# Performance work log

Hardware: AMD Instinct MI355X
Metric: run time of the kernel (lower is better)

The kernel has to match this reference:

```python
import jax, jax.numpy as jnp
import numpy as np
import math

N_HEADS = 16
D_MODEL = 1024
D_FF = 4096
MAX_REL = 32  # max_relative_position
LN_EPS = 1e-5


def _layernorm(x, g, b):
    m = jnp.mean(x, axis=-1, keepdims=True)
    v = jnp.var(x, axis=-1, keepdims=True)
    return (x - m) * jax.lax.rsqrt(v + LN_EPS) * g + b


def setup_inputs() -> dict:
    key = jax.random.key(0)
    ks = jax.random.split(key, 12)
    D, F = D_MODEL, D_FF
    gain = 1.0 / math.sqrt(2.0)
    xav = lambda k, o, i, g=1.0: jax.random.uniform(k, (o, i), jnp.float32, -1.0, 1.0) * (g * math.sqrt(6.0 / (o + i)))
    return {
        "x": jax.random.normal(ks[0], (2, 2048, D), jnp.float32),
        "wq": xav(ks[1], D, D, gain),
        "wk": xav(ks[2], D, D, gain),
        "wv": xav(ks[3], D, D, gain),
        "wo": xav(ks[4], D, D, gain),
        "wo_b": jnp.zeros((D,), jnp.float32),
        "rel_tab": jax.random.normal(ks[5], (2 * MAX_REL - 1, N_HEADS), jnp.float32) * 0.02,
        "ln1_g": jnp.ones((D,), jnp.float32),
        "ln1_b": jnp.zeros((D,), jnp.float32),
        "ln2_g": jnp.ones((D,), jnp.float32),
        "ln2_b": jnp.zeros((D,), jnp.float32),
        "w1": xav(ks[6], F, D),
        "b1": jnp.zeros((F,), jnp.float32),
        "w2": xav(ks[7], D, F),
        "b2": jnp.zeros((D,), jnp.float32),
    }


def reference(x, wq, wk, wv, wo, wo_b, rel_tab, ln1_g, ln1_b, ln2_g, ln2_b, w1, b1, w2, b2):
    B, S, D = x.shape
    H = N_HEADS
    dk = D // H

    def proj(w):  # torch Linear: x @ w.T, then split heads -> [B,H,S,dk]
        return (x @ w.T).reshape(B, S, H, dk).transpose(0, 2, 1, 3)

    q, k, v = proj(wq), proj(wk), proj(wv)

    # Rotary embeddings (per-head dim), exact interleave-to-block formula from source
    t = jnp.arange(S, dtype=jnp.float32)
    inv_freq = 1.0 / (10000.0 ** (jnp.arange(0, dk, 2, dtype=jnp.float32) / dk))
    freqs = t[:, None] * inv_freq[None, :]  # [S, dk/2]
    cos, sin = jnp.cos(freqs), jnp.sin(freqs)

    def rope(z):
        z1, z2 = z[..., ::2], z[..., 1::2]  # [B,H,S,dk/2]
        return jnp.concatenate([z1 * cos - z2 * sin, z1 * sin + z2 * cos], axis=-1)

    q, k = rope(q), rope(k)

    # Manual attention with learned relative-position bias
    scores = jnp.einsum("bhqd,bhkd->bhqk", q, k) / math.sqrt(dk)
    rel = jnp.arange(S)[:, None] - jnp.arange(S)[None, :]
    rel = jnp.clip(rel, -(MAX_REL - 1), MAX_REL - 1) + (MAX_REL - 1)
    bias = rel_tab[rel]  # [S,S,H]
    scores = scores + jnp.transpose(bias, (2, 0, 1))[None]  # [1,H,S,S]
    attn = jax.nn.softmax(scores, axis=-1)
    o = jnp.einsum("bhqk,bhkd->bhqd", attn, v).transpose(0, 2, 1, 3).reshape(B, S, D)
    o = o @ wo.T + wo_b

    # Post-norm residual block
    h = _layernorm(x + o, ln1_g, ln1_b)
    f = jax.nn.gelu(h @ w1.T + b1, approximate=False) @ w2.T + b2
    return _layernorm(h + f, ln2_g, ln2_b)
```

## Files before the change

### kernel.cpp

```cpp
#include <hip/hip_runtime.h>
#include <stdint.h>

#define MB (1ull << 20)
typedef unsigned short u16;
typedef __attribute__((ext_vector_type(8))) short bf16x8;
typedef __attribute__((ext_vector_type(4))) float f32x4;

__device__ __forceinline__ float b2f(u16 u) {
  union { unsigned int i; float f; } c; c.i = ((unsigned int)u) << 16; return c.f;
}
__device__ __forceinline__ u16 f2b(float f) {
  union { float f; unsigned int i; } c; c.f = f;
  unsigned int r = c.i + 0x7fffu + ((c.i >> 16) & 1u);
  return (u16)(r >> 16);
}
__device__ __forceinline__ void gload16(const void* g, void* l) {
  __builtin_amdgcn_global_load_lds(
      (const __attribute__((address_space(1))) void*)g,
      (__attribute__((address_space(3))) void*)l, 16, 0, 0);
}

__global__ __launch_bounds__(256) void f2b_kernel(const float* __restrict__ in,
                                                  u16* __restrict__ out, int n) {
  int i = (blockIdx.x * 256 + threadIdx.x) * 4;
  if (i + 3 >= n) { for (int j = 0; j < 4 && i + j < n; j++) out[i + j] = f2b(in[i + j]); return; }
  float4 v = *(const float4*)(in + i);
  uint2 o;
  o.x = (unsigned)f2b(v.x) | ((unsigned)f2b(v.y) << 16);
  o.y = (unsigned)f2b(v.z) | ((unsigned)f2b(v.w) << 16);
  *(uint2*)(out + i) = o;
}

template<int EPI, int BM>
__global__ __launch_bounds__(256) void gemm_bt(
    const u16* __restrict__ A, const u16* __restrict__ B,
    u16* __restrict__ C, const float* __restrict__ bias,
    int M, int N, int K)
{
  constexpr int MT = BM / 32;
  __shared__ __align__(16) u16 As[BM * 64];
  __shared__ __align__(16) u16 Bs[128 * 64];
  const int tid = threadIdx.x;
  const int lane = tid & 63, wave = tid >> 6;
  const int lr = lane & 15, lg = lane >> 4;
  const int wm = wave >> 1, wn = wave & 1;

  const int nwg = gridDim.x * gridDim.y;
  const int id = blockIdx.y * gridDim.x + blockIdx.x;
  const int nid = (id & 7) * (nwg >> 3) + (id >> 3);
  const int bx = nid % gridDim.x, by = nid / gridDim.x;

  const int srow = tid >> 3;
  const int scsw = ((tid & 7) * 8) ^ ((srow & 7) << 3);
  const size_t abase = (size_t)(by * BM + srow) * K + scsw;
  const size_t bbase = (size_t)(bx * 128 + srow) * K + scsw;

  int aoff[MT][2], boff[4][2];
  #pragma unroll
  for (int mt = 0; mt < MT; mt++) {
    int row = wm * (BM / 2) + mt * 16 + lr;
    #pragma unroll
    for (int kk = 0; kk < 2; kk++)
      aoff[mt][kk] = row * 64 + ((kk * 32 + lg * 8) ^ ((row & 7) << 3));
  }
  #pragma unroll
  for (int nt = 0; nt < 4; nt++) {
    int row = wn * 64 + nt * 16 + lr;
    #pragma unroll
    for (int kk = 0; kk < 2; kk++)
      boff[nt][kk] = row * 64 + ((kk * 32 + lg * 8) ^ ((row & 7) << 3));
  }

  f32x4 acc[MT][4];
  #pragma unroll
  for (int i = 0; i < MT; i++)
    #pragma unroll
    for (int j = 0; j < 4; j++) acc[i][j] = (f32x4){0.f, 0.f, 0.f, 0.f};

  for (int k0 = 0; k0 < K; k0 += 64) {
    __syncthreads();
    #pragma unroll
    for (int h = 0; h < MT; h++)
      gload16(A + abase + (size_t)(h * 32) * K + k0, &As[h * 2048 + tid * 8]);
    #pragma unroll
    for (int h = 0; h < 4; h++)
      gload16(B + bbase + (size_t)(h * 32) * K + k0, &Bs[h * 2048 + tid * 8]);
    __syncthreads();
    #pragma unroll
    for (int kk = 0; kk < 2; kk++) {
      bf16x8 af[MT], bfr[4];
      #pragma unroll
      for (int mt = 0; mt < MT; mt++) af[mt] = *(const bf16x8*)&As[aoff[mt][kk]];
      #pragma unroll
      for (int nt = 0; nt < 4; nt++) bfr[nt] = *(const bf16x8*)&Bs[boff[nt][kk]];
      #pragma unroll
      for (int mt = 0; mt < MT; mt++)
        #pragma unroll
        for (int nt = 0; nt < 4; nt++)
          acc[mt][nt] = __builtin_amdgcn_mfma_f32_16x16x32_bf16(af[mt], bfr[nt], acc[mt][nt], 0, 0, 0);
    }
  }

  #pragma unroll
  for (int mt = 0; mt < MT; mt++)
    #pragma unroll
    for (int nt = 0; nt < 4; nt++) {
      const int row = by * BM + wm * (BM / 2) + mt * 16 + lg * 4;
      const int col = bx * 128 + wn * 64 + nt * 16 + lr;
      const float bv = (EPI >= 1) ? bias[col] : 0.f;
      #pragma unroll
      for (int r = 0; r < 4; r++) {
        float x = acc[mt][nt][r] + bv;
        if (EPI == 2) x = 0.5f * x * (1.f + erff(x * 0.70710678118654752f));
        C[(size_t)(row + r) * N + col] = f2b(x);
      }
    }
}

__global__ __launch_bounds__(256) void rope_kernel(
    const u16* __restrict__ qp, const u16* __restrict__ kp, int stride,
    u16* __restrict__ qr, u16* __restrict__ kr)
{
  const int gid = blockIdx.x * 4 + (threadIdx.x >> 6);
  const int lane = threadIdx.x & 63;
  const int s = gid & 2047;
  const int bh = gid >> 11;
  const int h = bh & 15, b = bh >> 4;
  const int j = lane & 31;
  const float inv = exp2f(-(float)j * (13.287712379549449f / 32.0f));
  float sn, cs;
  sincosf((float)s * inv, &sn, &cs);
  const size_t base = (size_t)(b * 2048 + s) * stride + h * 64;
  float q1 = b2f(qp[base + 2 * j]), q2 = b2f(qp[base + 2 * j + 1]);
  float k1 = b2f(kp[base + 2 * j]), k2 = b2f(kp[base + 2 * j + 1]);
  float qo = (lane < 32) ? (q1 * cs - q2 * sn) : (q1 * sn + q2 * cs);
  float ko = (lane < 32) ? (k1 * cs - k2 * sn) : (k1 * sn + k2 * cs);
  qr[(size_t)gid * 64 + lane] = f2b(qo);
  kr[(size_t)gid * 64 + lane] = f2b(ko);
}

__global__ __launch_bounds__(256) void vtrans_kernel(
    const u16* __restrict__ vp, int stride, u16* __restrict__ vT)
{
  __shared__ u16 t[64][65];
  const int sc = blockIdx.x & 31;
  const int bh = blockIdx.x >> 5;
  const int h = bh & 15, b = bh >> 4;
  const int tid = threadIdx.x;
  #pragma unroll
  for (int i = 0; i < 16; i++) {
    int idx = i * 256 + tid;
    int sl = idx >> 6, d = idx & 63;
    t[sl][d] = vp[(size_t)(b * 2048 + sc * 64 + sl) * stride + h * 64 + d];
  }
  __syncthreads();
  #pragma unroll
  for (int i = 0; i < 16; i++) {
    int idx = i * 256 + tid;
    int d = idx >> 6, sl = idx & 63;
    vT[((size_t)bh * 64 + d) * 2048 + sc * 64 + sl] = t[sl][d];
  }
}

__global__ __launch_bounds__(256) void attn_kernel(
    const u16* __restrict__ qr, const u16* __restrict__ kr,
    const u16* __restrict__ vT, const float* __restrict__ rel_tab,
    u16* __restrict__ o)
{
  __shared__ __align__(16) u16 Ks[64 * 64];
  __shared__ __align__(16) u16 Vs[64 * 64];
  __shared__ __align__(16) u16 Ps[4][16 * 64];
  __shared__ float bias_s[64];

  const int tid = threadIdx.x;
  const int lane = tid & 63, wave = tid >> 6;
  const int lr = lane & 15, lg = lane >> 4;

  const int id = blockIdx.x;
  const int nid = (id & 7) * 128 + (id >> 3);
  const int bh = nid >> 5, qc = nid & 31;
  const int h = bh & 15, b = bh >> 4;
  const int q0 = qc * 64 + wave * 16;

  if (tid < 63) bias_s[tid] = rel_tab[tid * 16 + h] * 1.4426950408889634f;

  const u16* qb = qr + (size_t)bh * 2048 * 64;
  const u16* kb = kr + (size_t)bh * 2048 * 64;
  const u16* vb = vT + (size_t)bh * 64 * 2048;

  bf16x8 qf[2];
  qf[0] = *(const bf16x8*)(qb + (size_t)(q0 + lr) * 64 + lg * 8);
  qf[1] = *(const bf16x8*)(qb + (size_t)(q0 + lr) * 64 + 32 + lg * 8);

  const int srow = tid >> 3;
  const int scsw = ((tid & 7) * 8) ^ ((srow & 7) << 3);

  int koff[4][2], poff[2];
  #pragma unroll
  for (int nt = 0; nt < 4; nt++)
    #pragma unroll
    for (int ks = 0; ks < 2; ks++)
      koff[nt][ks] = (nt * 16 + lr) * 64 + ((ks * 32 + lg * 8) ^ ((lr & 7) << 3));
  #pragma unroll
  for (int ks = 0; ks < 2; ks++)
    poff[ks] = lr * 64 + ((ks * 32 + lg * 8) ^ ((lr & 7) << 3));

  float mrow[4], lpart[4];
  #pragma unroll
  for (int r = 0; r < 4; r++) { mrow[r] = -1e30f; lpart[r] = 0.f; }
  f32x4 oacc[4];
  #pragma unroll
  for (int nt = 0; nt < 4; nt++) oacc[nt] = (f32x4){0.f, 0.f, 0.f, 0.f};

  const float SC = 0.18033688011112042f;

  for (int kc = 0; kc < 32; kc++) {
    const int k0 = kc * 64;
    __syncthreads();
    #pragma unroll
    for (int hh = 0; hh < 2; hh++) {
      gload16(kb + (size_t)(k0 + hh * 32 + srow) * 64 + scsw, &Ks[hh * 2048 + tid * 8]);
      gload16(vb + (size_t)(hh * 32 + srow) * 2048 + k0 + scsw, &Vs[hh * 2048 + tid * 8]);
    }
    __syncthreads();

    f32x4 sacc[4];
    #pragma unroll
    for (int nt = 0; nt < 4; nt++) sacc[nt] = (f32x4){0.f, 0.f, 0.f, 0.f};
    #pragma unroll
    for (int ks = 0; ks < 2; ks++)
      #pragma unroll
      for (int nt = 0; nt < 4; nt++) {
        bf16x8 kf = *(const bf16x8*)&Ks[koff[nt][ks]];
        sacc[nt] = __builtin_amdgcn_mfma_f32_16x16x32_bf16(qf[ks], kf, sacc[nt], 0, 0, 0);
      }

    float sv[4][4];
    const int dmin = q0 - k0 - 63, dmax = q0 + 15 - k0;
    if (dmin >= 31 || dmax <= -31) {
      const float c = bias_s[dmin >= 31 ? 62 : 0];
      #pragma unroll
      for (int nt = 0; nt < 4; nt++)
        #pragma unroll
        for (int r = 0; r < 4; r++) sv[nt][r] = sacc[nt][r] * SC + c;
    } else {
      #pragma unroll
      for (int nt = 0; nt < 4; nt++)
        #pragma unroll
        for (int r = 0; r < 4; r++) {
          int d = (q0 + lg * 4 + r) - (k0 + nt * 16 + lr);
          d = d < -31 ? -31 : (d > 31 ? 31 : d);
          sv[nt][r] = sacc[nt][r] * SC + bias_s[d + 31];
        }
    }

    float rm[4];
    #pragma unroll
    for (int r = 0; r < 4; r++) {
      float m = fmaxf(fmaxf(sv[0][r], sv[1][r]), fmaxf(sv[2][r], sv[3][r]));
      m = fmaxf(m, __shfl_xor(m, 1));
      m = fmaxf(m, __shfl_xor(m, 2));
      m = fmaxf(m, __shfl_xor(m, 4));
      m = fmaxf(m, __shfl_xor(m, 8));
      rm[r] = m;
    }
    int defer = (rm[0] <= mrow[0] + 11.5f) & (rm[1] <= mrow[1] + 11.5f) &
                (rm[2] <= mrow[2] + 11.5f) & (rm[3] <= mrow[3] + 11.5f);
    if (!__all(defer)) {
      #pragma unroll
      for (int r = 0; r < 4; r++) {
        float mnew = fmaxf(mrow[r], rm[r]);
        float sc = exp2f(mrow[r] - mnew);
        lpart[r] *= sc;
        #pragma unroll
        for (int nt = 0; nt < 4; nt++) oacc[nt][r] *= sc;
        mrow[r] = mnew;
      }
    }
    #pragma unroll
    for (int r = 0; r < 4; r++) {
      const int prow = lg * 4 + r;
      const int sw = (prow & 7) << 3;
      #pragma unroll
      for (int nt = 0; nt < 4; nt++) {
        float p = exp2f(sv[nt][r] - mrow[r]);
        lpart[r] += p;
        Ps[wave][prow * 64 + ((nt * 16 + lr) ^ sw)] = f2b(p);
      }
    }
    #pragma unroll
    for (int ks = 0; ks < 2; ks++) {
      bf16x8 pf = *(const bf16x8*)&Ps[wave][poff[ks]];
      #pragma unroll
      for (int nt = 0; nt < 4; nt++) {
        bf16x8 vf = *(const bf16x8*)&Vs[koff[nt][ks]];
        oacc[nt] = __builtin_amdgcn_mfma_f32_16x16x32_bf16(pf, vf, oacc[nt], 0, 0, 0);
      }
    }
  }

  #pragma unroll
  for (int r = 0; r < 4; r++) {
    float l = lpart[r];
    l += __shfl_xor(l, 1); l += __shfl_xor(l, 2);
    l += __shfl_xor(l, 4); l += __shfl_xor(l, 8);
    lpart[r] = 1.0f / l;
  }
  #pragma unroll
  for (int nt = 0; nt < 4; nt++)
    #pragma unroll
    for (int r = 0; r < 4; r++) {
      int qa = q0 + lg * 4 + r;
      int d = nt * 16 + lr;
      o[(size_t)(b * 2048 + qa) * 1024 + h * 64 + d] = f2b(oacc[nt][r] * lpart[r]);
    }
}

__global__ __launch_bounds__(256) void ln1_kernel(
    const float* __restrict__ x, const u16* __restrict__ ao,
    const float* __restrict__ g, const float* __restrict__ bta,
    u16* __restrict__ hb)
{
  const int row = blockIdx.x, tid = threadIdx.x;
  const int wave = tid >> 6, lane = tid & 63;
  float v[4]; float s = 0.f, s2 = 0.f;
  #pragma unroll
  for (int j = 0; j < 4; j++) {
    int c = tid + j * 256;
    float t = x[(size_t)row * 1024 + c] + b2f(ao[(size_t)row * 1024 + c]);
    v[j] = t; s += t; s2 += t * t;
  }
  #pragma unroll
  for (int off = 32; off >= 1; off >>= 1) { s += __shfl_down(s, off); s2 += __shfl_down(s2, off); }
  __shared__ float rs[4], rs2[4];
  if (lane == 0) { rs[wave] = s; rs2[wave] = s2; }
  __syncthreads();
  s = rs[0] + rs[1] + rs[2] + rs[3];
  s2 = rs2[0] + rs2[1] + rs2[2] + rs2[3];
  float mean = s * (1.f / 1024.f);
  float var = s2 * (1.f / 1024.f) - mean * mean;
  float inv = rsqrtf(var + 1e-5f);
  #pragma unroll
  for (int j = 0; j < 4; j++) {
    int c = tid + j * 256;
    hb[(size_t)row * 1024 + c] = f2b((v[j] - mean) * inv * g[c] + bta[c]);
  }
}

__global__ __launch_bounds__(256) void ln2_kernel(
    const u16* __restrict__ hb, const u16* __restrict__ fb,
    const float* __restrict__ g, const float* __restrict__ bta,
    float* __restrict__ out)
{
  const int row = blockIdx.x, tid = threadIdx.x;
  const int wave = tid >> 6, lane = tid & 63;
  float v[4]; float s = 0.f, s2 = 0.f;
  #pragma unroll
  for (int j = 0; j < 4; j++) {
    int c = tid + j * 256;
    float t = b2f(hb[(size_t)row * 1024 + c]) + b2f(fb[(size_t)row * 1024 + c]);
    v[j] = t; s += t; s2 += t * t;
  }
  #pragma unroll
  for (int off = 32; off >= 1; off >>= 1) { s += __shfl_down(s, off); s2 += __shfl_down(s2, off); }
  __shared__ float rs[4], rs2[4];
  if (lane == 0) { rs[wave] = s; rs2[wave] = s2; }
  __syncthreads();
  s = rs[0] + rs[1] + rs[2] + rs[3];
  s2 = rs2[0] + rs2[1] + rs2[2] + rs2[3];
  float mean = s * (1.f / 1024.f);
  float var = s2 * (1.f / 1024.f) - mean * mean;
  float inv = rsqrtf(var + 1e-5f);
  #pragma unroll
  for (int j = 0; j < 4; j++) {
    int c = tid + j * 256;
    out[(size_t)row * 1024 + c] = (v[j] - mean) * inv * g[c] + bta[c];
  }
}

extern "C" void kernel_launch(void* const* d_in, const int* in_sizes, int n_in,
                              void* d_out, int out_size, void* d_ws, size_t ws_size,
                              hipStream_t stream)
{
  const float* x    = (const float*)d_in[0];
  const float* wq   = (const float*)d_in[1];
  const float* wk   = (const float*)d_in[2];
  const float* wv   = (const float*)d_in[3];
  const float* wo   = (const float*)d_in[4];
  const float* wo_b = (const float*)d_in[5];
  const float* rel  = (const float*)d_in[6];
  const float* ln1g = (const float*)d_in[7];
  const float* ln1b = (const float*)d_in[8];
  const float* ln2g = (const float*)d_in[9];
  const float* ln2b = (const float*)d_in[10];
  const float* w1   = (const float*)d_in[11];
  const float* b1   = (const float*)d_in[12];
  const float* w2   = (const float*)d_in[13];
  const float* b2   = (const float*)d_in[14];
  float* out = (float*)d_out;
  char* w = (char*)d_ws;

  if (ws_size < (size_t)90 * MB) return;

  u16* xb    = (u16*)(w + 0 * MB);
  u16* wqkvb = (u16*)(w + 8 * MB);
  u16* wob   = (u16*)(w + 14 * MB);
  u16* w1b   = (u16*)(w + 16 * MB);
  u16* w2b   = (u16*)(w + 24 * MB);
  u16* qkv   = (u16*)(w + 32 * MB);
  u16* ob    = (u16*)(w + 32 * MB);
  u16* ao    = (u16*)(w + 40 * MB);
  u16* hb    = (u16*)(w + 48 * MB);
  u16* qrb   = (u16*)(w + 56 * MB);
  u16* krb   = (u16*)(w + 64 * MB);
  u16* vTb   = (u16*)(w + 72 * MB);
  u16* gb    = (u16*)(w + 56 * MB);
  u16* fb    = (u16*)(w + 0 * MB);

  const int M = 4096, D = 1024, F = 4096;

  f2b_kernel<<<dim3(M * D / 1024), 256, 0, stream>>>(x, xb, M * D);
  f2b_kernel<<<dim3(D * D / 1024), 256, 0, stream>>>(wq, wqkvb, D * D);
  f2b_kernel<<<dim3(D * D / 1024), 256, 0, stream>>>(wk, wqkvb + D * D, D * D);
  f2b_kernel<<<dim3(D * D / 1024), 256, 0, stream>>>(wv, wqkvb + 2 * D * D, D * D);
  f2b_kernel<<<dim3(D * D / 1024), 256, 0, stream>>>(wo, wob, D * D);
  f2b_kernel<<<dim3(F * D / 1024), 256, 0, stream>>>(w1, w1b, F * D);
  f2b_kernel<<<dim3(D * F / 1024), 256, 0, stream>>>(w2, w2b, D * F);

  gemm_bt<0, 128><<<dim3(3 * D / 128, M / 128), 256, 0, stream>>>(xb, wqkvb, qkv, nullptr, M, 3 * D, D);

  rope_kernel<<<dim3(16384), 256, 0, stream>>>(qkv, qkv + 1024, 3 * D, qrb, krb);
  vtrans_kernel<<<dim3(1024), 256, 0, stream>>>(qkv + 2048, 3 * D, vTb);

  attn_kernel<<<dim3(1024), 256, 0, stream>>>(qrb, krb, vTb, rel, ob);

  gemm_bt<1, 64><<<dim3(D / 128, M / 64), 256, 0, stream>>>(ob, wob, ao, wo_b, M, D, D);

  ln1_kernel<<<dim3(M), 256, 0, stream>>>(x, ao, ln1g, ln1b, hb);

  gemm_bt<2, 128><<<dim3(F / 128, M / 128), 256, 0, stream>>>(hb, w1b, gb, b1, M, F, D);

  gemm_bt<1, 64><<<dim3(D / 128, M / 64), 256, 0, stream>>>(gb, w2b, fb, b2, M, D, F);

  ln2_kernel<<<dim3(M), 256, 0, stream>>>(hb, fb, ln2g, ln2b, out);
}
```

Baseline: 311.3 us.

## Double-buffer attention K/V, keep P in registers, fuse casts, precompute RoPE table

The attention kernel now double-buffers K/V tiles in LDS, prefetching the next chunk while computing the current one. It computes the transposed score tile so each lane owns one query row, which makes the per-row max and sum scalars. P is packed with v_cvt_pk_bf16_f32 and passed to the PV MFMA through ds_bpermute instead of an LDS round trip, with s_setprio around the MFMA sections. Separately, the seven fp32-to-bf16 conversions are merged into one launch and RoPE cos/sin come from a precomputed table, with paired 32-bit loads. This trades more LDS per block and lane shuffles for fewer barriers and fewer LDS writes; the attention loop drops the second __syncthreads, and it is not obvious that the async global_load_lds prefetch is guaranteed complete before the next iteration reads it.

```diff
diff --git a/kernel.cpp b/kernel.cpp
--- a/kernel.cpp
+++ b/kernel.cpp
@@ -20,15 +20,37 @@
       (__attribute__((address_space(3))) void*)l, 16, 0, 0);
 }
 
-__global__ __launch_bounds__(256) void f2b_kernel(const float* __restrict__ in,
-                                                  u16* __restrict__ out, int n) {
-  int i = (blockIdx.x * 256 + threadIdx.x) * 4;
-  if (i + 3 >= n) { for (int j = 0; j < 4 && i + j < n; j++) out[i + j] = f2b(in[i + j]); return; }
-  float4 v = *(const float4*)(in + i);
-  uint2 o;
-  o.x = (unsigned)f2b(v.x) | ((unsigned)f2b(v.y) << 16);
-  o.y = (unsigned)f2b(v.z) | ((unsigned)f2b(v.w) << 16);
-  *(uint2*)(out + i) = o;
+__global__ __launch_bounds__(256) void f2b_all(
+    const float* __restrict__ x, const float* __restrict__ wq, const float* __restrict__ wk,
+    const float* __restrict__ wv, const float* __restrict__ wo, const float* __restrict__ w1,
+    const float* __restrict__ w2,
+    u16* __restrict__ xb, u16* __restrict__ wqkvb, u16* __restrict__ wob,
+    u16* __restrict__ w1b, u16* __restrict__ w2b)
+{
+  int bid = blockIdx.x;
+  const float* src; u16* dst;
+  if (bid < 4096)       { src = x;  dst = xb; }
+  else if (bid < 5120)  { src = wq; dst = wqkvb;           bid -= 4096; }
+  else if (bid < 6144)  { src = wk; dst = wqkvb + 1048576; bid -= 5120; }
+  else if (bid < 7168)  { src = wv; dst = wqkvb + 2097152; bid -= 6144; }
+  else if (bid < 8192)  { src = wo; dst = wob;             bid -= 7168; }
+  else if (bid < 12288) { src = w1; dst = w1b;             bid -= 8192; }
+  else                  { src = w2; dst = w2b;             bid -= 12288; }
+  int i = (bid * 256 + threadIdx.x) * 4;
+  float4 v = *(const float4*)(src + i);
+  uint2 ov;
+  ov.x = (unsigned)f2b(v.x) | ((unsigned)f2b(v.y) << 16);
+  ov.y = (unsigned)f2b(v.z) | ((unsigned)f2b(v.w) << 16);
+  *(uint2*)(dst + i) = ov;
+}
+
+__global__ __launch_bounds__(256) void rope_tab_kernel(float2* __restrict__ tab) {
+  int idx = blockIdx.x * 256 + threadIdx.x;
+  int s = idx >> 5, j = idx & 31;
+  float inv = exp2f(-(float)j * (13.287712379549449f / 32.0f));
+  float sn, cs;
+  sincosf((float)s * inv, &sn, &cs);
+  tab[idx] = make_float2(cs, sn);
 }
 
 template<int EPI, int BM>
@@ -119,7 +141,7 @@
 
 __global__ __launch_bounds__(256) void rope_kernel(
     const u16* __restrict__ qp, const u16* __restrict__ kp, int stride,
-    u16* __restrict__ qr, u16* __restrict__ kr)
+    const float2* __restrict__ tab, u16* __restrict__ qr, u16* __restrict__ kr)
 {
   const int gid = blockIdx.x * 4 + (threadIdx.x >> 6);
   const int lane = threadIdx.x & 63;
@@ -127,12 +149,13 @@
   const int bh = gid >> 11;
   const int h = bh & 15, b = bh >> 4;
   const int j = lane & 31;
-  const float inv = exp2f(-(float)j * (13.287712379549449f / 32.0f));
-  float sn, cs;
-  sincosf((float)s * inv, &sn, &cs);
+  float2 t = tab[s * 32 + j];
+  const float cs = t.x, sn = t.y;
   const size_t base = (size_t)(b * 2048 + s) * stride + h * 64;
-  float q1 = b2f(qp[base + 2 * j]), q2 = b2f(qp[base + 2 * j + 1]);
-  float k1 = b2f(kp[base + 2 * j]), k2 = b2f(kp[base + 2 * j + 1]);
+  unsigned int qv = *(const unsigned int*)(qp + base + 2 * j);
+  unsigned int kv = *(const unsigned int*)(kp + base + 2 * j);
+  float q1 = b2f((u16)qv), q2 = b2f((u16)(qv >> 16));
+  float k1 = b2f((u16)kv), k2 = b2f((u16)(kv >> 16));
   float qo = (lane < 32) ? (q1 * cs - q2 * sn) : (q1 * sn + q2 * cs);
   float ko = (lane < 32) ? (k1 * cs - k2 * sn) : (k1 * sn + k2 * cs);
   qr[(size_t)gid * 64 + lane] = f2b(qo);
@@ -167,9 +190,8 @@
     const u16* __restrict__ vT, const float* __restrict__ rel_tab,
     u16* __restrict__ o)
 {
-  __shared__ __align__(16) u16 Ks[64 * 64];
-  __shared__ __align__(16) u16 Vs[64 * 64];
-  __shared__ __align__(16) u16 Ps[4][16 * 64];
+  __shared__ __align__(16) u16 Ks[2][64 * 64];
+  __shared__ __align__(16) u16 Vs[2][64 * 64];
   __shared__ float bias_s[64];
 
   const int tid = threadIdx.x;
@@ -195,125 +217,144 @@
   const int srow = tid >> 3;
   const int scsw = ((tid & 7) * 8) ^ ((srow & 7) << 3);
 
-  int koff[4][2], poff[2];
+  int koff[4][2];
   #pragma unroll
   for (int nt = 0; nt < 4; nt++)
     #pragma unroll
     for (int ks = 0; ks < 2; ks++)
       koff[nt][ks] = (nt * 16 + lr) * 64 + ((ks * 32 + lg * 8) ^ ((lr & 7) << 3));
-  #pragma unroll
-  for (int ks = 0; ks < 2; ks++)
-    poff[ks] = lr * 64 + ((ks * 32 + lg * 8) ^ ((lr & 7) << 3));
-
-  float mrow[4], lpart[4];
-  #pragma unroll
-  for (int r = 0; r < 4; r++) { mrow[r] = -1e30f; lpart[r] = 0.f; }
+
+  #pragma unroll
+  for (int hh = 0; hh < 2; hh++) {
+    gload16(kb + (size_t)(hh * 32 + srow) * 64 + scsw, &Ks[0][hh * 2048 + tid * 8]);
+    gload16(vb + (size_t)(hh * 32 + srow) * 2048 + scsw, &Vs[0][hh * 2048 + tid * 8]);
+  }
+
+  float mrow = -1e30f, lpart = 0.f;
   f32x4 oacc[4];
   #pragma unroll
   for (int nt = 0; nt < 4; nt++) oacc[nt] = (f32x4){0.f, 0.f, 0.f, 0.f};
 
   const float SC = 0.18033688011112042f;
-
+  const int idx_lo = 4 * (lr + 16 * ((lg & 1) * 2));
+  const int idx_hi = idx_lo + 64;
+  const bool hiSel = (lg >= 2);
+
+  int cur = 0;
   for (int kc = 0; kc < 32; kc++) {
     const int k0 = kc * 64;
     __syncthreads();
-    #pragma unroll
-    for (int hh = 0; hh < 2; hh++) {
-      gload16(kb + (size_t)(k0 + hh * 32 + srow) * 64 + scsw, &Ks[hh * 2048 + tid * 8]);
-      gload16(vb + (size_t)(hh * 32 + srow) * 2048 + k0 + scsw, &Vs[hh * 2048 + tid * 8]);
-    }
-    __syncthreads();
+    if (kc < 31) {
+      const int kn = k0 + 64;
+      #pragma unroll
+      for (int hh = 0; hh < 2; hh++) {
+        gload16(kb + (size_t)(kn + hh * 32 + srow) * 64 + scsw, &Ks[cur ^ 1][hh * 2048 + tid * 8]);
+        gload16(vb + (size_t)(hh * 32 + srow) * 2048 + kn + scsw, &Vs[cur ^ 1][hh * 2048 + tid * 8]);
+      }
+    }
+    const u16* Kc = Ks[cur];
+    const u16* Vc = Vs[cur];
 
     f32x4 sacc[4];
     #pragma unroll
     for (int nt = 0; nt < 4; nt++) sacc[nt] = (f32x4){0.f, 0.f, 0.f, 0.f};
+    __builtin_amdgcn_s_setprio(1);
     #pragma unroll
     for (int ks = 0; ks < 2; ks++)
       #pragma unroll
       for (int nt = 0; nt < 4; nt++) {
-        bf16x8 kf = *(const bf16x8*)&Ks[koff[nt][ks]];
-        sacc[nt] = __builtin_amdgcn_mfma_f32_16x16x32_bf16(qf[ks], kf, sacc[nt], 0, 0, 0);
+        bf16x8 kf = *(const bf16x8*)&Kc[koff[nt][ks]];
+        sacc[nt] = __builtin_amdgcn_mfma_f32_16x16x32_bf16(kf, qf[ks], sacc[nt], 0, 0, 0);
       }
-
-    float sv[4][4];
+    __builtin_amdgcn_s_setprio(0);
+
+    float p[4][4];
     const int dmin = q0 - k0 - 63, dmax = q0 + 15 - k0;
     if (dmin >= 31 || dmax <= -31) {
       const float c = bias_s[dmin >= 31 ? 62 : 0];
       #pragma unroll
       for (int nt = 0; nt < 4; nt++)
         #pragma unroll
-        for (int r = 0; r < 4; r++) sv[nt][r] = sacc[nt][r] * SC + c;
+        for (int r = 0; r < 4; r++) p[nt][r] = sacc[nt][r] * SC + c;
     } else {
       #pragma unroll
       for (int nt = 0; nt < 4; nt++)
         #pragma unroll
         for (int r = 0; r < 4; r++) {
-          int d = (q0 + lg * 4 + r) - (k0 + nt * 16 + lr);
+          int d = (q0 + lr) - (k0 + nt * 16 + lg * 4 + r);
           d = d < -31 ? -31 : (d > 31 ? 31 : d);
-          sv[nt][r] = sacc[nt][r] * SC + bias_s[d + 31];
+          p[nt][r] = sacc[nt][r] * SC + bias_s[d + 31];
         }
     }
 
-    float rm[4];
-    #pragma unroll
-    for (int r = 0; r < 4; r++) {
-      float m = fmaxf(fmaxf(sv[0][r], sv[1][r]), fmaxf(sv[2][r], sv[3][r]));
-      m = fmaxf(m, __shfl_xor(m, 1));
-      m = fmaxf(m, __shfl_xor(m, 2));
-      m = fmaxf(m, __shfl_xor(m, 4));
-      m = fmaxf(m, __shfl_xor(m, 8));
-      rm[r] = m;
-    }
-    int defer = (rm[0] <= mrow[0] + 11.5f) & (rm[1] <= mrow[1] + 11.5f) &
-                (rm[2] <= mrow[2] + 11.5f) & (rm[3] <= mrow[3] + 11.5f);
-    if (!__all(defer)) {
-      #pragma unroll
-      for (int r = 0; r < 4; r++) {
-        float mnew = fmaxf(mrow[r], rm[r]);
-        float sc = exp2f(mrow[r] - mnew);
-        lpart[r] *= sc;
-        #pragma unroll
-        for (int nt = 0; nt < 4; nt++) oacc[nt][r] *= sc;
-        mrow[r] = mnew;
+    float rm = p[0][0];
+    #pragma unroll
+    for (int nt = 0; nt < 4; nt++)
+      #pragma unroll
+      for (int r = 0; r < 4; r++) rm = fmaxf(rm, p[nt][r]);
+    rm = fmaxf(rm, __shfl_xor(rm, 16));
+    rm = fmaxf(rm, __shfl_xor(rm, 32));
+
+    if (!__all(rm <= mrow + 11.5f)) {
+      float mnew = fmaxf(mrow, rm);
+      float sc = exp2f(mrow - mnew);
+      lpart *= sc;
+      #pragma unroll
+      for (int nt = 0; nt < 4; nt++) oacc[nt] *= sc;
+      mrow = mnew;
+    }
+
+    unsigned int pk[4][2];
+    #pragma unroll
+    for (int nt = 0; nt < 4; nt++)
+      #pragma unroll
+      for (int i = 0; i < 2; i++) {
+        float pa = exp2f(p[nt][2 * i] - mrow);
+        float pb = exp2f(p[nt][2 * i + 1] - mrow);
+        lpart += pa + pb;
+        unsigned int pr;
+        asm("v_cvt_pk_bf16_f32 %0, %1, %2" : "=v"(pr) : "v"(pa), "v"(pb));
+        pk[nt][i] = pr;
       }
-    }
-    #pragma unroll
-    for (int r = 0; r < 4; r++) {
-      const int prow = lg * 4 + r;
-      const int sw = (prow & 7) << 3;
+
+    __builtin_amdgcn_s_setprio(1);
+    #pragma unroll
+    for (int ks = 0; ks < 2; ks++) {
+      int w0a = __builtin_amdgcn_ds_bpermute(idx_lo, (int)pk[ks * 2][0]);
+      int w0b = __builtin_amdgcn_ds_bpermute(idx_lo, (int)pk[ks * 2 + 1][0]);
+      int w1a = __builtin_amdgcn_ds_bpermute(idx_lo, (int)pk[ks * 2][1]);
+      int w1b = __builtin_amdgcn_ds_bpermute(idx_lo, (int)pk[ks * 2 + 1][1]);
+      int w2a = __builtin_amdgcn_ds_bpermute(idx_hi, (int)pk[ks * 2][0]);
+      int w2b = __builtin_amdgcn_ds_bpermute(idx_hi, (int)pk[ks * 2 + 1][0]);
+      int w3a = __builtin_amdgcn_ds_bpermute(idx_hi, (int)pk[ks * 2][1]);
+      int w3b = __builtin_amdgcn_ds_bpermute(idx_hi, (int)pk[ks * 2 + 1][1]);
+      int4 bw;
+      bw.x = hiSel ? w0b : w0a;
+      bw.y = hiSel ? w1b : w1a;
+      bw.z = hiSel ? w2b : w2a;
+      bw.w = hiSel ? w3b : w3a;
+      bf16x8 pf = *(bf16x8*)&bw;
       #pragma unroll
       for (int nt = 0; nt < 4; nt++) {
-        float p = exp2f(sv[nt][r] - mrow[r]);
-        lpart[r] += p;
-        Ps[wave][prow * 64 + ((nt * 16 + lr) ^ sw)] = f2b(p);
+        bf16x8 vf = *(const bf16x8*)&Vc[koff[nt][ks]];
+        oacc[nt] = __builtin_amdgcn_mfma_f32_16x16x32_bf16(vf, pf, oacc[nt], 0, 0, 0);
       }
     }
-    #pragma unroll
-    for (int ks = 0; ks < 2; ks++) {
-      bf16x8 pf = *(const bf16x8*)&Ps[wave][poff[ks]];
-      #pragma unroll
-      for (int nt = 0; nt < 4; nt++) {
-        bf16x8 vf = *(const bf16x8*)&Vs[koff[nt][ks]];
-        oacc[nt] = __builtin_amdgcn_mfma_f32_16x16x32_bf16(pf, vf, oacc[nt], 0, 0, 0);
-      }
-    }
-  }
-
-  #pragma unroll
-  for (int r = 0; r < 4; r++) {
-    float l = lpart[r];
-    l += __shfl_xor(l, 1); l += __shfl_xor(l, 2);
-    l += __shfl_xor(l, 4); l += __shfl_xor(l, 8);
-    lpart[r] = 1.0f / l;
-  }
-  #pragma unroll
-  for (int nt = 0; nt < 4; nt++)
-    #pragma unroll
-    for (int r = 0; r < 4; r++) {
-      int qa = q0 + lg * 4 + r;
-      int d = nt * 16 + lr;
-      o[(size_t)(b * 2048 + qa) * 1024 + h * 64 + d] = f2b(oacc[nt][r] * lpart[r]);
-    }
+    __builtin_amdgcn_s_setprio(0);
+    cur ^= 1;
+  }
+
+  lpart += __shfl_xor(lpart, 16);
+  lpart += __shfl_xor(lpart, 32);
+  const float inv = 1.0f / lpart;
+  const size_t obase = (size_t)(b * 2048 + q0 + lr) * 1024 + h * 64;
+  #pragma unroll
+  for (int nt = 0; nt < 4; nt++) {
+    uint2 st;
+    st.x = (unsigned)f2b(oacc[nt][0] * inv) | ((unsigned)f2b(oacc[nt][1] * inv) << 16);
+    st.y = (unsigned)f2b(oacc[nt][2] * inv) | ((unsigned)f2b(oacc[nt][3] * inv) << 16);
+    *(uint2*)(o + obase + nt * 16 + lg * 4) = st;
+  }
 }
 
 __global__ __launch_bounds__(256) void ln1_kernel(
@@ -416,20 +457,17 @@
   u16* vTb   = (u16*)(w + 72 * MB);
   u16* gb    = (u16*)(w + 56 * MB);
   u16* fb    = (u16*)(w + 0 * MB);
+  float2* tab = (float2*)(w + 88 * MB);
 
   const int M = 4096, D = 1024, F = 4096;
 
-  f2b_kernel<<<dim3(M * D / 1024), 256, 0, stream>>>(x, xb, M * D);
-  f2b_kernel<<<dim3(D * D / 1024), 256, 0, stream>>>(wq, wqkvb, D * D);
-  f2b_kernel<<<dim3(D * D / 1024), 256, 0, stream>>>(wk, wqkvb + D * D, D * D);
-  f2b_kernel<<<dim3(D * D / 1024), 256, 0, stream>>>(wv, wqkvb + 2 * D * D, D * D);
-  f2b_kernel<<<dim3(D * D / 1024), 256, 0, stream>>>(wo, wob, D * D);
-  f2b_kernel<<<dim3(F * D / 1024), 256, 0, stream>>>(w1, w1b, F * D);
-  f2b_kernel<<<dim3(D * F / 1024), 256, 0, stream>>>(w2, w2b, D * F);
+  rope_tab_kernel<<<dim3(256), 256, 0, stream>>>(tab);
+  f2b_all<<<dim3(16384), 256, 0, stream>>>(x, wq, wk, wv, wo, w1, w2,
+                                           xb, wqkvb, wob, w1b, w2b);
 
   gemm_bt<0, 128><<<dim3(3 * D / 128, M / 128), 256, 0, stream>>>(xb, wqkvb, qkv, nullptr, M, 3 * D, D);
 
-  rope_kernel<<<dim3(16384), 256, 0, stream>>>(qkv, qkv + 1024, 3 * D, qrb, krb);
+  rope_kernel<<<dim3(16384), 256, 0, stream>>>(qkv, qkv + 1024, 3 * D, tab, qrb, krb);
   vtrans_kernel<<<dim3(1024), 256, 0, stream>>>(qkv + 2048, 3 * D, vTb);
 
   attn_kernel<<<dim3(1024), 256, 0, stream>>>(qrb, krb, vTb, rel, ob);
```

Result: faster. 290.7 us (-6.6%).
